# Performance work log

Measured on AMD Instinct MI355X. Metric: run time of the kernel, lower is better.

The kernel has to match this reference:

```python
import jax, jax.numpy as jnp
import numpy as np

N_VOX = 500_000
C = 128
HID = 4 * C
RES = 128  # voxel grid resolution
K_OFFS = 27


def _build_sparse_coords_and_neighbors(seed=0):
    rng = np.random.default_rng(seed)
    lin = rng.choice(RES ** 3, size=N_VOX, replace=False)
    z = lin // (RES * RES)
    y = (lin // RES) % RES
    x = lin % RES
    # padded grid (RES+2)^3 so boundary lookups are in-bounds
    P = RES + 2
    grid = -np.ones(P * P * P, dtype=np.int64)
    z1, y1, x1 = z + 1, y + 1, x + 1
    grid[z1 * P * P + y1 * P + x1] = np.arange(N_VOX)
    offs = np.array([[dz, dy, dx] for dz in (-1, 0, 1) for dy in (-1, 0, 1) for dx in (-1, 0, 1)], dtype=np.int64)  # [27,3]
    nz = z1[:, None] + offs[None, :, 0]
    ny = y1[:, None] + offs[None, :, 1]
    nx = x1[:, None] + offs[None, :, 2]
    nbr = grid[nz * P * P + ny * P + nx]  # [N,27], -1 if neighbor voxel inactive
    return nbr.astype(np.int32)


def setup_inputs() -> dict:
    key = jax.random.key(0)
    ks = jax.random.split(key, 8)
    nbr = _build_sparse_coords_and_neighbors()
    scale = 0.02
    return {
        "feats": jax.random.normal(ks[0], (N_VOX, C), jnp.float32),
        "neighbor_idx": jnp.asarray(nbr),
        "conv_w": jax.random.normal(ks[1], (K_OFFS, C, C), jnp.float32) * scale,
        "conv_b": jax.random.normal(ks[2], (C,), jnp.float32) * scale,
        "ln_g": jnp.ones((C,), jnp.float32),
        "ln_b": jnp.zeros((C,), jnp.float32),
        "w1": jax.random.normal(ks[3], (C, HID), jnp.float32) * scale,
        "b1": jax.random.normal(ks[4], (HID,), jnp.float32) * scale,
        "w2": jax.random.normal(ks[5], (HID, C), jnp.float32) * scale,
        "b2": jax.random.normal(ks[6], (C,), jnp.float32) * scale,
    }


def _forward(feats, neighbor_idx, conv_w, conv_b, ln_g, ln_b, w1, b1, w2, b2):
    n, c = feats.shape
    # submanifold sparse conv3d: pad a zero row for missing (-1) neighbors
    f_pad = jnp.concatenate([feats, jnp.zeros((1, c), feats.dtype)], axis=0)
    idx = jnp.where(neighbor_idx < 0, n, neighbor_idx)  # [N,27]
    h = jnp.broadcast_to(conv_b, (n, c))
    for k in range(K_OFFS):  # fixed small kernel-offset loop; per-offset gather + GEMM
        h = h + f_pad[idx[:, k]] @ conv_w[k]
    # LayerNorm32 (fp32 math), eps=1e-6, affine
    h32 = h.astype(jnp.float32)
    mu = h32.mean(-1, keepdims=True)
    var = h32.var(-1, keepdims=True)
    hn = ((h32 - mu) * jax.lax.rsqrt(var + 1e-6) * ln_g + ln_b).astype(feats.dtype)
    # MLP: Linear -> SiLU -> Linear
    m = jax.nn.silu(hn @ w1 + b1) @ w2 + b2
    # residual h + x on sparse feats
    return m + feats


def reference(feats, neighbor_idx, conv_w, conv_b, ln_g, ln_b, w1, b1, w2, b2):
    return _forward(feats, neighbor_idx, conv_w, conv_b, ln_g, ln_b, w1, b1, w2, b2)
```

## Files before the change

kernel.cpp:

```cpp
#include <hip/hip_runtime.h>
#include <stdint.h>

#define NVOX 500000
#define NPAD 500224
#define ZERO_OFF (NVOX * 128)

typedef float  f32x4  __attribute__((ext_vector_type(4)));
typedef short  short8 __attribute__((ext_vector_type(8)));

__device__ __forceinline__ short f2bf(float x){
  unsigned u = __float_as_uint(x);
  unsigned r = (u + 0x7fffu + ((u >> 16) & 1u)) >> 16;
  return (short)r;
}

__device__ __forceinline__ void gload_lds16(const void* g, void* l){
  __builtin_amdgcn_global_load_lds(
      (const __attribute__((address_space(1))) unsigned int*)(uintptr_t)g,
      (__attribute__((address_space(3))) unsigned int*)(unsigned int)(uintptr_t)l,
      16, 0, 0);
}

__global__ void cast_feats_kernel(const float* __restrict__ f, short* __restrict__ t){
  long i = ((long)blockIdx.x * 256 + threadIdx.x) * 8;
  float4 a = *(const float4*)(f + i);
  float4 b = *(const float4*)(f + i + 4);
  short8 o = { f2bf(a.x), f2bf(a.y), f2bf(a.z), f2bf(a.w),
               f2bf(b.x), f2bf(b.y), f2bf(b.z), f2bf(b.w) };
  *(short8*)(t + i) = o;
}

__global__ void prep_nbr_kernel(const int* __restrict__ nbr, int* __restrict__ nbrT){
  __shared__ int lds_n[6912];
  const int tid = threadIdx.x;
  const long base = (long)blockIdx.x * 6912;
  #pragma unroll
  for (int i = 0; i < 27; i++){
    long g = base + i*256 + tid;
    lds_n[i*256 + tid] = (g < (long)NVOX*27) ? nbr[g] : -1;
  }
  __syncthreads();
  const int row = blockIdx.x * 256 + tid;
  #pragma unroll
  for (int k = 0; k < 27; k++){
    int id = lds_n[tid*27 + k];
    nbrT[(size_t)k*NPAD + row] = (id < 0 ? NVOX : id) * 128;
  }
}

__global__ void prep_weights_kernel(const float* __restrict__ cw, const float* __restrict__ w1,
                                    const float* __restrict__ w2,
                                    short* __restrict__ cw_sw, short* __restrict__ w1_sw,
                                    short* __restrict__ w2_sw){
  int t = blockIdx.x * 256 + threadIdx.x;
  if (t < 55296){
    int k = t >> 11, rem = t & 2047;
    int nf = rem >> 8, ks = (rem >> 6) & 3, l = rem & 63;
    int g = l >> 4, c = l & 15;
    short8 o;
    #pragma unroll
    for (int j = 0; j < 8; j++){
      int kk = ks*32 + g*8 + j;
      o[j] = f2bf(cw[(k*128 + kk)*128 + nf*16 + c]);
    }
    *(short8*)(cw_sw + (size_t)t*8) = o;
  } else if (t < 63488){
    int u = t - 55296;
    int nf = u >> 8, ks = (u >> 6) & 3, l = u & 63;
    int g = l >> 4, c = l & 15;
    short8 o;
    #pragma unroll
    for (int j = 0; j < 8; j++){
      int kk = ks*32 + g*8 + j;
      o[j] = f2bf(w1[kk*512 + nf*16 + c]);
    }
    *(short8*)(w1_sw + (size_t)u*8) = o;
  } else {
    int u = t - 63488;
    int ch = u >> 10, rem = u & 1023;
    int nf = rem >> 7, ks2 = (rem >> 6) & 1, l = u & 63;
    int g = l >> 4, c = l & 15;
    short8 o;
    #pragma unroll
    for (int j = 0; j < 8; j++){
      int k = ch*64 + ks2*32 + g*8 + j;
      o[j] = f2bf(w2[k*128 + nf*16 + c]);
    }
    *(short8*)(w2_sw + (size_t)u*8) = o;
  }
}

__global__ __launch_bounds__(256, 2)
void conv_ln_pf_kernel(const short* __restrict__ table, const int* __restrict__ nbrT,
                       const short* __restrict__ cw_sw,
                       const float* __restrict__ conv_b, const float* __restrict__ ln_g,
                       const float* __restrict__ ln_b, short* __restrict__ hn16){
  __shared__ __align__(16) short lds_b[2][16384];
  const int tid = threadIdx.x;
  const int lane = tid & 63, wv = tid >> 6;
  const int l15 = lane & 15, lg = lane >> 4;
  const int rowbase = blockIdx.x * 256 + wv * 64;
  const int rowi = rowbase + l15;

  f32x4 acc[4][8];
  #pragma unroll
  for (int m = 0; m < 4; m++)
    #pragma unroll
    for (int n = 0; n < 8; n++)
      acc[m][n] = f32x4{0.f, 0.f, 0.f, 0.f};

  int idx_c[4], idx_n[4];
  #pragma unroll
  for (int m = 0; m < 4; m++) idx_c[m] = nbrT[rowi + m*16];
  #pragma unroll
  for (int m = 0; m < 4; m++) idx_n[m] = nbrT[NPAD + rowi + m*16];
  short8 afp[2][4];
  #pragma unroll
  for (int ks = 0; ks < 2; ks++)
    #pragma unroll
    for (int m = 0; m < 4; m++)
      afp[ks][m] = *(const short8*)(table + (size_t)(unsigned)idx_c[m] + ks*32 + lg*8);
  {
    const char* src = (const char*)cw_sw;
    char* dst = (char*)&lds_b[0][0];
    #pragma unroll
    for (int i = 0; i < 8; i++){ int off = i*4096 + tid*16; gload_lds16(src+off, dst+off); }
  }

  for (int k = 0; k < 27; k++){
    const int buf = k & 1;
    __syncthreads();
    short8 af2[4], af3[4];
    #pragma unroll
    for (int m = 0; m < 4; m++)
      af2[m] = *(const short8*)(table + (size_t)(unsigned)idx_c[m] + 64 + lg*8);
    #pragma unroll
    for (int m = 0; m < 4; m++)
      af3[m] = *(const short8*)(table + (size_t)(unsigned)idx_c[m] + 96 + lg*8);
    int idx_n2[4];
    #pragma unroll
    for (int m = 0; m < 4; m++)
      idx_n2[m] = (k + 2 < 27) ? nbrT[(size_t)(k+2)*NPAD + rowi + m*16] : ZERO_OFF;
    if (k + 1 < 27){
      const char* src = (const char*)cw_sw + (size_t)(k+1)*32768;
      char* dst = (char*)&lds_b[buf ^ 1][0];
      #pragma unroll
      for (int i = 0; i < 8; i++){ int off = i*4096 + tid*16; gload_lds16(src+off, dst+off); }
    }

    const short* bbase = &lds_b[buf][0];
    #pragma unroll
    for (int ks = 0; ks < 2; ks++){
      #pragma unroll
      for (int n = 0; n < 8; n++){
        short8 b = *(const short8*)(bbase + ((n*4 + ks)*64 + lane)*8);
        #pragma unroll
        for (int m = 0; m < 4; m++)
          acc[m][n] = __builtin_amdgcn_mfma_f32_16x16x32_bf16(afp[ks][m], b, acc[m][n], 0, 0, 0);
      }
    }
    short8 afp_n[2][4];
    #pragma unroll
    for (int ks = 0; ks < 2; ks++)
      #pragma unroll
      for (int m = 0; m < 4; m++)
        afp_n[ks][m] = *(const short8*)(table + (size_t)(unsigned)idx_n[m] + ks*32 + lg*8);
    #pragma unroll
    for (int n = 0; n < 8; n++){
      short8 b = *(const short8*)(bbase + ((n*4 + 2)*64 + lane)*8);
      #pragma unroll
      for (int m = 0; m < 4; m++)
        acc[m][n] = __builtin_amdgcn_mfma_f32_16x16x32_bf16(af2[m], b, acc[m][n], 0, 0, 0);
    }
    #pragma unroll
    for (int n = 0; n < 8; n++){
      short8 b = *(const short8*)(bbase + ((n*4 + 3)*64 + lane)*8);
      #pragma unroll
      for (int m = 0; m < 4; m++)
        acc[m][n] = __builtin_amdgcn_mfma_f32_16x16x32_bf16(af3[m], b, acc[m][n], 0, 0, 0);
    }
    #pragma unroll
    for (int m = 0; m < 4; m++){
      afp[0][m] = afp_n[0][m];
      afp[1][m] = afp_n[1][m];
      idx_c[m] = idx_n[m];
      idx_n[m] = idx_n2[m];
    }
  }

  float cb[8], g8[8], be[8];
  #pragma unroll
  for (int n = 0; n < 8; n++){
    cb[n] = conv_b[n*16 + l15];
    g8[n] = ln_g[n*16 + l15];
    be[n] = ln_b[n*16 + l15];
  }
  #pragma unroll
  for (int m = 0; m < 4; m++){
    #pragma unroll
    for (int r = 0; r < 4; r++){
      float s = 0.f, s2 = 0.f;
      #pragma unroll
      for (int n = 0; n < 8; n++){
        float h = acc[m][n][r] + cb[n];
        acc[m][n][r] = h;
        s += h; s2 += h*h;
      }
      #pragma unroll
      for (int msk = 1; msk < 16; msk <<= 1){
        s  += __shfl_xor(s,  msk);
        s2 += __shfl_xor(s2, msk);
      }
      float mu  = s  * 0.0078125f;
      float var = s2 * 0.0078125f - mu*mu;
      float rs  = rsqrtf(var + 1e-6f);
      int row = rowbase + m*16 + lg*4 + r;
      if (row < NVOX){
        #pragma unroll
        for (int n = 0; n < 8; n++){
          float hv = (acc[m][n][r] - mu) * rs * g8[n] + be[n];
          hn16[(size_t)row*128 + n*16 + l15] = f2bf(hv);
        }
      }
    }
  }
}

template<bool TBL>
__global__ __launch_bounds__(256, 2)
void conv_ln_kernel(const short* __restrict__ table, const float* __restrict__ feats,
                    const int* __restrict__ nbr, const short* __restrict__ cw_sw,
                    const float* __restrict__ conv_b, const float* __restrict__ ln_g,
                    const float* __restrict__ ln_b, short* __restrict__ hn16){
  __shared__ __align__(16) short lds_b[2][16384];
  const int tid = threadIdx.x;
  const int lane = tid & 63, wv = tid >> 6;
  const int l15 = lane & 15, lg = lane >> 4;
  const int rowbase = blockIdx.x * 256 + wv * 64;

  f32x4 acc[4][8];
  #pragma unroll
  for (int m = 0; m < 4; m++)
    #pragma unroll
    for (int n = 0; n < 8; n++)
      acc[m][n] = f32x4{0.f, 0.f, 0.f, 0.f};

  {
    const char* src = (const char*)cw_sw;
    char* dst = (char*)&lds_b[0][0];
    #pragma unroll
    for (int i = 0; i < 8; i++){ int off = i*4096 + tid*16; gload_lds16(src+off, dst+off); }
  }

  for (int k = 0; k < 27; k++){
    const int buf = k & 1;
    __syncthreads();
    if (k + 1 < 27){
      const char* src = (const char*)cw_sw + (size_t)(k+1)*32768;
      char* dst = (char*)&lds_b[buf ^ 1][0];
      #pragma unroll
      for (int i = 0; i < 8; i++){ int off = i*4096 + tid*16; gload_lds16(src+off, dst+off); }
    }
    int idxr[4];
    #pragma unroll
    for (int m = 0; m < 4; m++){
      int row = rowbase + m*16 + l15;
      row = row < NVOX ? row : NVOX - 1;
      int id = nbr[row*27 + k];
      idxr[m] = TBL ? (id < 0 ? NVOX : id) : id;
    }
    const short* bbase = &lds_b[buf][0];
    #pragma unroll
    for (int ks = 0; ks < 4; ks++){
      short8 af[4];
      #pragma unroll
      for (int m = 0; m < 4; m++){
        if constexpr (TBL){
          af[m] = *(const short8*)(table + (size_t)idxr[m]*128 + ks*32 + lg*8);
        } else {
          if (idxr[m] < 0){
            af[m] = short8{0,0,0,0,0,0,0,0};
          } else {
            const float* p = feats + (size_t)idxr[m]*128 + ks*32 + lg*8;
            float4 x = *(const float4*)p;
            float4 y = *(const float4*)(p + 4);
            af[m] = short8{ f2bf(x.x), f2bf(x.y), f2bf(x.z), f2bf(x.w),
                            f2bf(y.x), f2bf(y.y), f2bf(y.z), f2bf(y.w) };
          }
        }
      }
      #pragma unroll
      for (int n = 0; n < 8; n++){
        short8 b = *(const short8*)(bbase + ((n*4 + ks)*64 + lane)*8);
        #pragma unroll
        for (int m = 0; m < 4; m++)
          acc[m][n] = __builtin_amdgcn_mfma_f32_16x16x32_bf16(af[m], b, acc[m][n], 0, 0, 0);
      }
    }
  }

  float cb[8], g8[8], be[8];
  #pragma unroll
  for (int n = 0; n < 8; n++){
    cb[n] = conv_b[n*16 + l15];
    g8[n] = ln_g[n*16 + l15];
    be[n] = ln_b[n*16 + l15];
  }
  #pragma unroll
  for (int m = 0; m < 4; m++){
    #pragma unroll
    for (int r = 0; r < 4; r++){
      float s = 0.f, s2 = 0.f;
      #pragma unroll
      for (int n = 0; n < 8; n++){
        float h = acc[m][n][r] + cb[n];
        acc[m][n][r] = h;
        s += h; s2 += h*h;
      }
      #pragma unroll
      for (int msk = 1; msk < 16; msk <<= 1){
        s  += __shfl_xor(s,  msk);
        s2 += __shfl_xor(s2, msk);
      }
      float mu  = s  * 0.0078125f;
      float var = s2 * 0.0078125f - mu*mu;
      float rs  = rsqrtf(var + 1e-6f);
      int row = rowbase + m*16 + lg*4 + r;
      if (row < NVOX){
        #pragma unroll
        for (int n = 0; n < 8; n++){
          float hv = (acc[m][n][r] - mu) * rs * g8[n] + be[n];
          hn16[(size_t)row*128 + n*16 + l15] = f2bf(hv);
        }
      }
    }
  }
}

__global__ __launch_bounds__(256, 2)
void mlp_kernel(const short* __restrict__ hn16, const float* __restrict__ feats,
                const short* __restrict__ w1_sw, const short* __restrict__ w2_sw,
                const float* __restrict__ b1, const float* __restrict__ b2,
                float* __restrict__ out){
  __shared__ __align__(16) short lds_w[2][16384];
  __shared__ __align__(16) short lds_act[4*2048];
  const int tid = threadIdx.x;
  const int lane = tid & 63, wv = tid >> 6;
  const int l15 = lane & 15, lg = lane >> 4;
  const int rowbase = blockIdx.x * 128 + wv * 32;
  short* actw = &lds_act[wv * 2048];

  f32x4 acc2[2][8];
  #pragma unroll
  for (int m = 0; m < 2; m++)
    #pragma unroll
    for (int n = 0; n < 8; n++)
      acc2[m][n] = f32x4{0.f, 0.f, 0.f, 0.f};

  int rowg[2];
  #pragma unroll
  for (int m = 0; m < 2; m++){
    int row = rowbase + m*16 + l15;
    rowg[m] = row < NVOX ? row : NVOX - 1;
  }

  short8 a1[4][2];
  #pragma unroll
  for (int ks = 0; ks < 4; ks++)
    #pragma unroll
    for (int m = 0; m < 2; m++)
      a1[ks][m] = *(const short8*)(hn16 + (size_t)rowg[m]*128 + ks*32 + lg*8);

  {
    const char* s1 = (const char*)w1_sw;
    const char* s2 = (const char*)w2_sw;
    char* dst = (char*)&lds_w[0][0];
    #pragma unroll
    for (int i = 0; i < 4; i++){ int off = i*4096 + tid*16; gload_lds16(s1+off, dst+off); }
    #pragma unroll
    for (int i = 0; i < 4; i++){ int off = i*4096 + tid*16; gload_lds16(s2+off, dst+16384+off); }
  }

  for (int ch = 0; ch < 8; ch++){
    const int buf = ch & 1;
    __syncthreads();
    if (ch + 1 < 8){
      const char* s1 = (const char*)w1_sw + (size_t)(ch+1)*16384;
      const char* s2 = (const char*)w2_sw + (size_t)(ch+1)*16384;
      char* dst = (char*)&lds_w[buf ^ 1][0];
      #pragma unroll
      for (int i = 0; i < 4; i++){ int off = i*4096 + tid*16; gload_lds16(s1+off, dst+off); }
      #pragma unroll
      for (int i = 0; i < 4; i++){ int off = i*4096 + tid*16; gload_lds16(s2+off, dst+16384+off); }
    }
    const short* w1c = &lds_w[buf][0];
    const short* w2c = &lds_w[buf][8192];

    #pragma unroll
    for (int n = 0; n < 4; n++){
      f32x4 p0 = f32x4{0.f,0.f,0.f,0.f};
      f32x4 p1 = f32x4{0.f,0.f,0.f,0.f};
      #pragma unroll
      for (int ks = 0; ks < 4; ks++){
        short8 b = *(const short8*)(w1c + ((n*4 + ks)*64 + lane)*8);
        p0 = __builtin_amdgcn_mfma_f32_16x16x32_bf16(a1[ks][0], b, p0, 0, 0, 0);
        p1 = __builtin_amdgcn_mfma_f32_16x16x32_bf16(a1[ks][1], b, p1, 0, 0, 0);
      }
      float bb1 = b1[ch*64 + n*16 + l15];
      #pragma unroll
      for (int r = 0; r < 4; r++){
        float x0 = p0[r] + bb1;
        float x1 = p1[r] + bb1;
        float s0 = x0 / (1.f + __expf(-x0));
        float s1 = x1 / (1.f + __expf(-x1));
        int r0 = lg*4 + r;
        int r1 = 16 + lg*4 + r;
        actw[(r0*64 + n*16 + l15) ^ ((r0 & 7) << 3)] = f2bf(s0);
        actw[(r1*64 + n*16 + l15) ^ ((r1 & 7) << 3)] = f2bf(s1);
      }
    }

    #pragma unroll
    for (int ks2 = 0; ks2 < 2; ks2++){
      short8 a2[2];
      #pragma unroll
      for (int m = 0; m < 2; m++){
        int rowloc = m*16 + l15;
        a2[m] = *(const short8*)(actw + ((rowloc*64 + ks2*32 + lg*8) ^ ((rowloc & 7) << 3)));
      }
      #pragma unroll
      for (int n = 0; n < 8; n++){
        short8 b = *(const short8*)(w2c + ((n*2 + ks2)*64 + lane)*8);
        #pragma unroll
        for (int m = 0; m < 2; m++)
          acc2[m][n] = __builtin_amdgcn_mfma_f32_16x16x32_bf16(a2[m], b, acc2[m][n], 0, 0, 0);
      }
    }
  }

  float bb2[8];
  #pragma unroll
  for (int n = 0; n < 8; n++) bb2[n] = b2[n*16 + l15];
  #pragma unroll
  for (int m = 0; m < 2; m++)
    #pragma unroll
    for (int n = 0; n < 8; n++)
      #pragma unroll
      for (int r = 0; r < 4; r++){
        int row = rowbase + m*16 + lg*4 + r;
        if (row < NVOX){
          size_t ci = (size_t)row*128 + n*16 + l15;
          out[ci] = acc2[m][n][r] + bb2[n] + feats[ci];
        }
      }
}

extern "C" void kernel_launch(void* const* d_in, const int* in_sizes, int n_in,
                              void* d_out, int out_size, void* d_ws, size_t ws_size,
                              hipStream_t stream){
  const float* feats = (const float*)d_in[0];
  const int*   nbr   = (const int*)  d_in[1];
  const float* cw    = (const float*)d_in[2];
  const float* cb    = (const float*)d_in[3];
  const float* lng   = (const float*)d_in[4];
  const float* lnb   = (const float*)d_in[5];
  const float* w1    = (const float*)d_in[6];
  const float* b1    = (const float*)d_in[7];
  const float* w2    = (const float*)d_in[8];
  const float* b2    = (const float*)d_in[9];
  float* out = (float*)d_out;

  char* ws = (char*)d_ws;
  const size_t TABLE_B = (size_t)(NVOX + 1) * 256;
  const size_t HN_B    = (size_t)NVOX * 256;
  const size_t CW_B    = 55296u * 16u;
  const size_t W1_B    = 8192u * 16u;
  const size_t W2_B    = 8192u * 16u;
  const size_t NBRT_B  = (size_t)27 * NPAD * 4;
  const size_t need_full = TABLE_B + HN_B + CW_B + W1_B + W2_B;
  const size_t need_pf   = need_full + NBRT_B;

  if (ws_size >= need_pf){
    short* table = (short*)ws;
    short* hn16  = (short*)(ws + TABLE_B);
    short* cw_sw = (short*)(ws + TABLE_B + HN_B);
    short* w1_sw = (short*)(ws + TABLE_B + HN_B + CW_B);
    short* w2_sw = (short*)(ws + TABLE_B + HN_B + CW_B + W1_B);
    int*   nbrT  = (int*)  (ws + need_full);

    cast_feats_kernel<<<31250, 256, 0, stream>>>(feats, table);
    hipMemsetAsync((void*)(table + (size_t)NVOX * 128), 0, 256, stream);
    prep_nbr_kernel<<<1954, 256, 0, stream>>>(nbr, nbrT);
    prep_weights_kernel<<<280, 256, 0, stream>>>(cw, w1, w2, cw_sw, w1_sw, w2_sw);
    conv_ln_pf_kernel<<<1954, 256, 0, stream>>>(table, nbrT, cw_sw, cb, lng, lnb, hn16);
    mlp_kernel<<<3907, 256, 0, stream>>>(hn16, feats, w1_sw, w2_sw, b1, b2, out);
  } else if (ws_size >= need_full){
    short* table = (short*)ws;
    short* hn16  = (short*)(ws + TABLE_B);
    short* cw_sw = (short*)(ws + TABLE_B + HN_B);
    short* w1_sw = (short*)(ws + TABLE_B + HN_B + CW_B);
    short* w2_sw = (short*)(ws + TABLE_B + HN_B + CW_B + W1_B);

    cast_feats_kernel<<<31250, 256, 0, stream>>>(feats, table);
    hipMemsetAsync((void*)(table + (size_t)NVOX * 128), 0, 256, stream);
    prep_weights_kernel<<<280, 256, 0, stream>>>(cw, w1, w2, cw_sw, w1_sw, w2_sw);
    conv_ln_kernel<true><<<1954, 256, 0, stream>>>(table, feats, nbr, cw_sw, cb, lng, lnb, hn16);
    mlp_kernel<<<3907, 256, 0, stream>>>(hn16, feats, w1_sw, w2_sw, b1, b2, out);
  } else {
    short* hn16  = (short*)ws;
    short* cw_sw = (short*)(ws + HN_B);
    short* w1_sw = (short*)(ws + HN_B + CW_B);
    short* w2_sw = (short*)(ws + HN_B + CW_B + W1_B);

    prep_weights_kernel<<<280, 256, 0, stream>>>(cw, w1, w2, cw_sw, w1_sw, w2_sw);
    conv_ln_kernel<false><<<1954, 256, 0, stream>>>(nullptr, feats, nbr, cw_sw, cb, lng, lnb, hn16);
    mlp_kernel<<<3907, 256, 0, stream>>>(hn16, feats, w1_sw, w2_sw, b1, b2, out);
  }
}
```

Baseline: 929.8 us.

## Split conv tile across wave pairs, halve LDS, raise occupancy

The conv+LayerNorm kernel now uses 128-row blocks, and two waves split the 128 output channels of each 64-row slab. This halves the accumulator registers and lets launch bounds request 4 blocks per CU. The weights are re-laid out into 16 KB half-offset chunks, so each offset is streamed in two halves through a 2x8192-short LDS buffer. LayerNorm row statistics are combined across the wave pair through shared memory. In exchange, every neighbour row is gathered twice (once per column half), the cross-offset A prefetch is dropped, and there are extra barriers per offset.

```diff
diff --git a/kernel.cpp b/kernel.cpp
--- a/kernel.cpp
+++ b/kernel.cpp
@@ -63,7 +63,8 @@
       int kk = ks*32 + g*8 + j;
       o[j] = f2bf(cw[(k*128 + kk)*128 + nf*16 + c]);
     }
-    *(short8*)(cw_sw + (size_t)t*8) = o;
+    size_t dst = (size_t)(k*2 + (ks >> 1))*8192 + (size_t)(nf*2 + (ks & 1))*512 + (size_t)l*8;
+    *(short8*)(cw_sw + dst) = o;
   } else if (t < 63488){
     int u = t - 55296;
     int nf = u >> 8, ks = (u >> 6) & 3, l = u & 63;
@@ -90,23 +91,26 @@
   }
 }
 
-__global__ __launch_bounds__(256, 2)
-void conv_ln_pf_kernel(const short* __restrict__ table, const int* __restrict__ nbrT,
+__global__ __launch_bounds__(256, 4)
+void conv_ln_v3_kernel(const short* __restrict__ table, const int* __restrict__ nbrT,
                        const short* __restrict__ cw_sw,
                        const float* __restrict__ conv_b, const float* __restrict__ ln_g,
                        const float* __restrict__ ln_b, short* __restrict__ hn16){
-  __shared__ __align__(16) short lds_b[2][16384];
+  __shared__ __align__(16) short lds_b[2][8192];
+  __shared__ float lds_s[128][2];
+  __shared__ float lds_s2[128][2];
   const int tid = threadIdx.x;
   const int lane = tid & 63, wv = tid >> 6;
+  const int wr = wv >> 1, wc = wv & 1;
   const int l15 = lane & 15, lg = lane >> 4;
-  const int rowbase = blockIdx.x * 256 + wv * 64;
+  const int rowbase = blockIdx.x * 128 + wr * 64;
   const int rowi = rowbase + l15;
 
-  f32x4 acc[4][8];
+  f32x4 acc[4][4];
   #pragma unroll
   for (int m = 0; m < 4; m++)
     #pragma unroll
-    for (int n = 0; n < 8; n++)
+    for (int n = 0; n < 4; n++)
       acc[m][n] = f32x4{0.f, 0.f, 0.f, 0.f};
 
   int idx_c[4], idx_n[4];
@@ -114,21 +118,46 @@
   for (int m = 0; m < 4; m++) idx_c[m] = nbrT[rowi + m*16];
   #pragma unroll
   for (int m = 0; m < 4; m++) idx_n[m] = nbrT[NPAD + rowi + m*16];
-  short8 afp[2][4];
-  #pragma unroll
-  for (int ks = 0; ks < 2; ks++)
-    #pragma unroll
-    for (int m = 0; m < 4; m++)
-      afp[ks][m] = *(const short8*)(table + (size_t)(unsigned)idx_c[m] + ks*32 + lg*8);
+
   {
     const char* src = (const char*)cw_sw;
     char* dst = (char*)&lds_b[0][0];
     #pragma unroll
-    for (int i = 0; i < 8; i++){ int off = i*4096 + tid*16; gload_lds16(src+off, dst+off); }
+    for (int i = 0; i < 4; i++){ int off = i*4096 + tid*16; gload_lds16(src+off, dst+off); }
   }
 
   for (int k = 0; k < 27; k++){
-    const int buf = k & 1;
+    __syncthreads();
+    short8 af0[4], af1[4];
+    #pragma unroll
+    for (int m = 0; m < 4; m++)
+      af0[m] = *(const short8*)(table + (size_t)(unsigned)idx_c[m] + lg*8);
+    #pragma unroll
+    for (int m = 0; m < 4; m++)
+      af1[m] = *(const short8*)(table + (size_t)(unsigned)idx_c[m] + 32 + lg*8);
+    {
+      const char* src = (const char*)cw_sw + (size_t)(k*2 + 1)*16384;
+      char* dst = (char*)&lds_b[1][0];
+      #pragma unroll
+      for (int i = 0; i < 4; i++){ int off = i*4096 + tid*16; gload_lds16(src+off, dst+off); }
+    }
+    {
+      const short* b0 = &lds_b[0][0];
+      #pragma unroll
+      for (int n = 0; n < 4; n++){
+        short8 b = *(const short8*)(b0 + (((wc*4 + n)*2 + 0)*64 + lane)*8);
+        #pragma unroll
+        for (int m = 0; m < 4; m++)
+          acc[m][n] = __builtin_amdgcn_mfma_f32_16x16x32_bf16(af0[m], b, acc[m][n], 0, 0, 0);
+      }
+      #pragma unroll
+      for (int n = 0; n < 4; n++){
+        short8 b = *(const short8*)(b0 + (((wc*4 + n)*2 + 1)*64 + lane)*8);
+        #pragma unroll
+        for (int m = 0; m < 4; m++)
+          acc[m][n] = __builtin_amdgcn_mfma_f32_16x16x32_bf16(af1[m], b, acc[m][n], 0, 0, 0);
+      }
+    }
     __syncthreads();
     short8 af2[4], af3[4];
     #pragma unroll
@@ -137,63 +166,43 @@
     #pragma unroll
     for (int m = 0; m < 4; m++)
       af3[m] = *(const short8*)(table + (size_t)(unsigned)idx_c[m] + 96 + lg*8);
+    if (k + 1 < 27){
+      const char* src = (const char*)cw_sw + (size_t)(k+1)*32768;
+      char* dst = (char*)&lds_b[0][0];
+      #pragma unroll
+      for (int i = 0; i < 4; i++){ int off = i*4096 + tid*16; gload_lds16(src+off, dst+off); }
+    }
     int idx_n2[4];
     #pragma unroll
     for (int m = 0; m < 4; m++)
       idx_n2[m] = (k + 2 < 27) ? nbrT[(size_t)(k+2)*NPAD + rowi + m*16] : ZERO_OFF;
-    if (k + 1 < 27){
-      const char* src = (const char*)cw_sw + (size_t)(k+1)*32768;
-      char* dst = (char*)&lds_b[buf ^ 1][0];
-      #pragma unroll
-      for (int i = 0; i < 8; i++){ int off = i*4096 + tid*16; gload_lds16(src+off, dst+off); }
-    }
-
-    const short* bbase = &lds_b[buf][0];
-    #pragma unroll
-    for (int ks = 0; ks < 2; ks++){
-      #pragma unroll
-      for (int n = 0; n < 8; n++){
-        short8 b = *(const short8*)(bbase + ((n*4 + ks)*64 + lane)*8);
+    {
+      const short* b1 = &lds_b[1][0];
+      #pragma unroll
+      for (int n = 0; n < 4; n++){
+        short8 b = *(const short8*)(b1 + (((wc*4 + n)*2 + 0)*64 + lane)*8);
         #pragma unroll
         for (int m = 0; m < 4; m++)
-          acc[m][n] = __builtin_amdgcn_mfma_f32_16x16x32_bf16(afp[ks][m], b, acc[m][n], 0, 0, 0);
-      }
-    }
-    short8 afp_n[2][4];
-    #pragma unroll
-    for (int ks = 0; ks < 2; ks++)
-      #pragma unroll
-      for (int m = 0; m < 4; m++)
-        afp_n[ks][m] = *(const short8*)(table + (size_t)(unsigned)idx_n[m] + ks*32 + lg*8);
-    #pragma unroll
-    for (int n = 0; n < 8; n++){
-      short8 b = *(const short8*)(bbase + ((n*4 + 2)*64 + lane)*8);
-      #pragma unroll
-      for (int m = 0; m < 4; m++)
-        acc[m][n] = __builtin_amdgcn_mfma_f32_16x16x32_bf16(af2[m], b, acc[m][n], 0, 0, 0);
-    }
-    #pragma unroll
-    for (int n = 0; n < 8; n++){
-      short8 b = *(const short8*)(bbase + ((n*4 + 3)*64 + lane)*8);
-      #pragma unroll
-      for (int m = 0; m < 4; m++)
-        acc[m][n] = __builtin_amdgcn_mfma_f32_16x16x32_bf16(af3[m], b, acc[m][n], 0, 0, 0);
-    }
-    #pragma unroll
-    for (int m = 0; m < 4; m++){
-      afp[0][m] = afp_n[0][m];
-      afp[1][m] = afp_n[1][m];
-      idx_c[m] = idx_n[m];
-      idx_n[m] = idx_n2[m];
-    }
-  }
-
-  float cb[8], g8[8], be[8];
-  #pragma unroll
-  for (int n = 0; n < 8; n++){
-    cb[n] = conv_b[n*16 + l15];
-    g8[n] = ln_g[n*16 + l15];
-    be[n] = ln_b[n*16 + l15];
+          acc[m][n] = __builtin_amdgcn_mfma_f32_16x16x32_bf16(af2[m], b, acc[m][n], 0, 0, 0);
+      }
+      #pragma unroll
+      for (int n = 0; n < 4; n++){
+        short8 b = *(const short8*)(b1 + (((wc*4 + n)*2 + 1)*64 + lane)*8);
+        #pragma unroll
+        for (int m = 0; m < 4; m++)
+          acc[m][n] = __builtin_amdgcn_mfma_f32_16x16x32_bf16(af3[m], b, acc[m][n], 0, 0, 0);
+      }
+    }
+    #pragma unroll
+    for (int m = 0; m < 4; m++){ idx_c[m] = idx_n[m]; idx_n[m] = idx_n2[m]; }
+  }
+
+  float cb[4], g4[4], be[4];
+  #pragma unroll
+  for (int n = 0; n < 4; n++){
+    cb[n] = conv_b[wc*64 + n*16 + l15];
+    g4[n] = ln_g[wc*64 + n*16 + l15];
+    be[n] = ln_b[wc*64 + n*16 + l15];
   }
   #pragma unroll
   for (int m = 0; m < 4; m++){
@@ -201,7 +210,7 @@
     for (int r = 0; r < 4; r++){
       float s = 0.f, s2 = 0.f;
       #pragma unroll
-      for (int n = 0; n < 8; n++){
+      for (int n = 0; n < 4; n++){
         float h = acc[m][n][r] + cb[n];
         acc[m][n][r] = h;
         s += h; s2 += h*h;
@@ -211,15 +220,27 @@
         s  += __shfl_xor(s,  msk);
         s2 += __shfl_xor(s2, msk);
       }
+      int rl = wr*64 + m*16 + lg*4 + r;
+      if (l15 == 0){ lds_s[rl][wc] = s; lds_s2[rl][wc] = s2; }
+    }
+  }
+  __syncthreads();
+  #pragma unroll
+  for (int m = 0; m < 4; m++){
+    #pragma unroll
+    for (int r = 0; r < 4; r++){
+      int rl = wr*64 + m*16 + lg*4 + r;
+      float s  = lds_s[rl][0]  + lds_s[rl][1];
+      float s2 = lds_s2[rl][0] + lds_s2[rl][1];
       float mu  = s  * 0.0078125f;
       float var = s2 * 0.0078125f - mu*mu;
       float rs  = rsqrtf(var + 1e-6f);
-      int row = rowbase + m*16 + lg*4 + r;
+      int row = blockIdx.x * 128 + rl;
       if (row < NVOX){
         #pragma unroll
-        for (int n = 0; n < 8; n++){
-          float hv = (acc[m][n][r] - mu) * rs * g8[n] + be[n];
-          hn16[(size_t)row*128 + n*16 + l15] = f2bf(hv);
+        for (int n = 0; n < 4; n++){
+          float hv = (acc[m][n][r] - mu) * rs * g4[n] + be[n];
+          hn16[(size_t)row*128 + wc*64 + n*16 + l15] = f2bf(hv);
         }
       }
     }
@@ -291,7 +312,7 @@
       }
       #pragma unroll
       for (int n = 0; n < 8; n++){
-        short8 b = *(const short8*)(bbase + ((n*4 + ks)*64 + lane)*8);
+        short8 b = *(const short8*)(bbase + (ks >> 1)*8192 + (((n*2 + (ks & 1))*64) + lane)*8);
         #pragma unroll
         for (int m = 0; m < 4; m++)
           acc[m][n] = __builtin_amdgcn_mfma_f32_16x16x32_bf16(af[m], b, acc[m][n], 0, 0, 0);
@@ -492,7 +513,7 @@
     hipMemsetAsync((void*)(table + (size_t)NVOX * 128), 0, 256, stream);
     prep_nbr_kernel<<<1954, 256, 0, stream>>>(nbr, nbrT);
     prep_weights_kernel<<<280, 256, 0, stream>>>(cw, w1, w2, cw_sw, w1_sw, w2_sw);
-    conv_ln_pf_kernel<<<1954, 256, 0, stream>>>(table, nbrT, cw_sw, cb, lng, lnb, hn16);
+    conv_ln_v3_kernel<<<3907, 256, 0, stream>>>(table, nbrT, cw_sw, cb, lng, lnb, hn16);
     mlp_kernel<<<3907, 256, 0, stream>>>(hn16, feats, w1_sw, w2_sw, b1, b2, out);
   } else if (ws_size >= need_full){
     short* table = (short*)ws;
```

After: 1.234 ms. 32.7% more time.

## Stream MLP weights from global into registers instead of LDS double buffering

Applied to the files above, without the earlier changes.

The MLP kernel stops staging W1/W2 chunks in shared memory with per-chunk __syncthreads. Each wave now loads its MFMA B fragments directly from global memory (L2-resident) into registers, prefetching the next fragment one step ahead. Hidden chunks grow from 64 to 128 columns, which doubles the per-wave activation LDS buffer and halves the chunk loop count. This removes block-wide barriers and cuts LDS use, which may raise occupancy. In exchange every wave issues redundant global loads for the weights and carries more registers for the prefetch buffers.

```diff
diff --git a/kernel.cpp b/kernel.cpp
--- a/kernel.cpp
+++ b/kernel.cpp
@@ -342,13 +342,12 @@
                 const short* __restrict__ w1_sw, const short* __restrict__ w2_sw,
                 const float* __restrict__ b1, const float* __restrict__ b2,
                 float* __restrict__ out){
-  __shared__ __align__(16) short lds_w[2][16384];
-  __shared__ __align__(16) short lds_act[4*2048];
+  __shared__ __align__(16) short lds_act[4*4096];
   const int tid = threadIdx.x;
   const int lane = tid & 63, wv = tid >> 6;
   const int l15 = lane & 15, lg = lane >> 4;
   const int rowbase = blockIdx.x * 128 + wv * 32;
-  short* actw = &lds_act[wv * 2048];
+  short* actw = &lds_act[wv * 4096];
 
   f32x4 acc2[2][8];
   #pragma unroll
@@ -371,42 +370,26 @@
     for (int m = 0; m < 2; m++)
       a1[ks][m] = *(const short8*)(hn16 + (size_t)rowg[m]*128 + ks*32 + lg*8);
 
-  {
-    const char* s1 = (const char*)w1_sw;
-    const char* s2 = (const char*)w2_sw;
-    char* dst = (char*)&lds_w[0][0];
-    #pragma unroll
-    for (int i = 0; i < 4; i++){ int off = i*4096 + tid*16; gload_lds16(s1+off, dst+off); }
-    #pragma unroll
-    for (int i = 0; i < 4; i++){ int off = i*4096 + tid*16; gload_lds16(s2+off, dst+16384+off); }
-  }
-
-  for (int ch = 0; ch < 8; ch++){
-    const int buf = ch & 1;
-    __syncthreads();
-    if (ch + 1 < 8){
-      const char* s1 = (const char*)w1_sw + (size_t)(ch+1)*16384;
-      const char* s2 = (const char*)w2_sw + (size_t)(ch+1)*16384;
-      char* dst = (char*)&lds_w[buf ^ 1][0];
-      #pragma unroll
-      for (int i = 0; i < 4; i++){ int off = i*4096 + tid*16; gload_lds16(s1+off, dst+off); }
-      #pragma unroll
-      for (int i = 0; i < 4; i++){ int off = i*4096 + tid*16; gload_lds16(s2+off, dst+16384+off); }
-    }
-    const short* w1c = &lds_w[buf][0];
-    const short* w2c = &lds_w[buf][8192];
-
-    #pragma unroll
-    for (int n = 0; n < 4; n++){
+  for (int ch = 0; ch < 4; ch++){
+    short8 bw[4], bn[4];
+    #pragma unroll
+    for (int ks = 0; ks < 4; ks++)
+      bw[ks] = *(const short8*)(w1_sw + (size_t)((ch*8 + 0)*4 + ks)*512 + lane*8);
+    #pragma unroll
+    for (int nf = 0; nf < 8; nf++){
+      if (nf < 7){
+        #pragma unroll
+        for (int ks = 0; ks < 4; ks++)
+          bn[ks] = *(const short8*)(w1_sw + (size_t)((ch*8 + nf + 1)*4 + ks)*512 + lane*8);
+      }
       f32x4 p0 = f32x4{0.f,0.f,0.f,0.f};
       f32x4 p1 = f32x4{0.f,0.f,0.f,0.f};
       #pragma unroll
       for (int ks = 0; ks < 4; ks++){
-        short8 b = *(const short8*)(w1c + ((n*4 + ks)*64 + lane)*8);
-        p0 = __builtin_amdgcn_mfma_f32_16x16x32_bf16(a1[ks][0], b, p0, 0, 0, 0);
-        p1 = __builtin_amdgcn_mfma_f32_16x16x32_bf16(a1[ks][1], b, p1, 0, 0, 0);
-      }
-      float bb1 = b1[ch*64 + n*16 + l15];
+        p0 = __builtin_amdgcn_mfma_f32_16x16x32_bf16(a1[ks][0], bw[ks], p0, 0, 0, 0);
+        p1 = __builtin_amdgcn_mfma_f32_16x16x32_bf16(a1[ks][1], bw[ks], p1, 0, 0, 0);
+      }
+      float bb1 = b1[ch*128 + nf*16 + l15];
       #pragma unroll
       for (int r = 0; r < 4; r++){
         float x0 = p0[r] + bb1;
@@ -415,26 +398,43 @@
         float s1 = x1 / (1.f + __expf(-x1));
         int r0 = lg*4 + r;
         int r1 = 16 + lg*4 + r;
-        actw[(r0*64 + n*16 + l15) ^ ((r0 & 7) << 3)] = f2bf(s0);
-        actw[(r1*64 + n*16 + l15) ^ ((r1 & 7) << 3)] = f2bf(s1);
-      }
-    }
-
-    #pragma unroll
-    for (int ks2 = 0; ks2 < 2; ks2++){
-      short8 a2[2];
+        actw[(r0*128 + nf*16 + l15) ^ ((r0 & 7) << 3)] = f2bf(s0);
+        actw[(r1*128 + nf*16 + l15) ^ ((r1 & 7) << 3)] = f2bf(s1);
+      }
+      #pragma unroll
+      for (int ks = 0; ks < 4; ks++) bw[ks] = bn[ks];
+    }
+
+    short8 a2h[4][2];
+    #pragma unroll
+    for (int ks2 = 0; ks2 < 4; ks2++)
       #pragma unroll
       for (int m = 0; m < 2; m++){
         int rowloc = m*16 + l15;
-        a2[m] = *(const short8*)(actw + ((rowloc*64 + ks2*32 + lg*8) ^ ((rowloc & 7) << 3)));
-      }
-      #pragma unroll
-      for (int n = 0; n < 8; n++){
-        short8 b = *(const short8*)(w2c + ((n*2 + ks2)*64 + lane)*8);
+        a2h[ks2][m] = *(const short8*)(actw + ((rowloc*128 + ks2*32 + lg*8) ^ ((rowloc & 7) << 3)));
+      }
+    short8 cw[4], cn[4];
+    #pragma unroll
+    for (int ks2 = 0; ks2 < 4; ks2++){
+      int ch64 = ch*2 + (ks2 >> 1), kk = ks2 & 1;
+      cw[ks2] = *(const short8*)(w2_sw + (size_t)(((ch64*8 + 0)*2 + kk)*64 + lane)*8);
+    }
+    #pragma unroll
+    for (int nfo = 0; nfo < 8; nfo++){
+      if (nfo < 7){
         #pragma unroll
-        for (int m = 0; m < 2; m++)
-          acc2[m][n] = __builtin_amdgcn_mfma_f32_16x16x32_bf16(a2[m], b, acc2[m][n], 0, 0, 0);
-      }
+        for (int ks2 = 0; ks2 < 4; ks2++){
+          int ch64 = ch*2 + (ks2 >> 1), kk = ks2 & 1;
+          cn[ks2] = *(const short8*)(w2_sw + (size_t)(((ch64*8 + nfo + 1)*2 + kk)*64 + lane)*8);
+        }
+      }
+      #pragma unroll
+      for (int ks2 = 0; ks2 < 4; ks2++){
+        acc2[0][nfo] = __builtin_amdgcn_mfma_f32_16x16x32_bf16(a2h[ks2][0], cw[ks2], acc2[0][nfo], 0, 0, 0);
+        acc2[1][nfo] = __builtin_amdgcn_mfma_f32_16x16x32_bf16(a2h[ks2][1], cw[ks2], acc2[1][nfo], 0, 0, 0);
+      }
+      #pragma unroll
+      for (int ks2 = 0; ks2 < 4; ks2++) cw[ks2] = cn[ks2];
     }
   }
 
```

New measurement: 1.027 ms. +10.4%, slower.

## Double MLP rows per wave and single-buffer weight chunks in LDS

Applied to the files above, without the earlier changes.

Each wave in the MLP kernel now processes 64 rows instead of 32, so every weight fragment read from LDS feeds four MFMAs instead of two. The grid is halved to match. The double-buffered weight prefetch is replaced by a single buffer loaded and then waited on with a barrier each chunk, which frees LDS for the larger activation tile. The cost is more registers per thread (more accumulators and a larger A tile), possible occupancy loss, and the weight loads no longer overlapping with compute.

```diff
diff --git a/kernel.cpp b/kernel.cpp
--- a/kernel.cpp
+++ b/kernel.cpp
@@ -342,97 +342,86 @@
                 const short* __restrict__ w1_sw, const short* __restrict__ w2_sw,
                 const float* __restrict__ b1, const float* __restrict__ b2,
                 float* __restrict__ out){
-  __shared__ __align__(16) short lds_w[2][16384];
-  __shared__ __align__(16) short lds_act[4*2048];
+  __shared__ __align__(16) short lds_w[16384];
+  __shared__ __align__(16) short lds_act[4*4096];
   const int tid = threadIdx.x;
   const int lane = tid & 63, wv = tid >> 6;
   const int l15 = lane & 15, lg = lane >> 4;
-  const int rowbase = blockIdx.x * 128 + wv * 32;
-  short* actw = &lds_act[wv * 2048];
-
-  f32x4 acc2[2][8];
-  #pragma unroll
-  for (int m = 0; m < 2; m++)
+  const int rowbase = blockIdx.x * 256 + wv * 64;
+  short* actw = &lds_act[wv * 4096];
+
+  f32x4 acc2[4][8];
+  #pragma unroll
+  for (int m = 0; m < 4; m++)
     #pragma unroll
     for (int n = 0; n < 8; n++)
       acc2[m][n] = f32x4{0.f, 0.f, 0.f, 0.f};
 
-  int rowg[2];
-  #pragma unroll
-  for (int m = 0; m < 2; m++){
+  int rowg[4];
+  #pragma unroll
+  for (int m = 0; m < 4; m++){
     int row = rowbase + m*16 + l15;
     rowg[m] = row < NVOX ? row : NVOX - 1;
   }
 
-  short8 a1[4][2];
+  short8 a1[4][4];
   #pragma unroll
   for (int ks = 0; ks < 4; ks++)
     #pragma unroll
-    for (int m = 0; m < 2; m++)
+    for (int m = 0; m < 4; m++)
       a1[ks][m] = *(const short8*)(hn16 + (size_t)rowg[m]*128 + ks*32 + lg*8);
 
-  {
-    const char* s1 = (const char*)w1_sw;
-    const char* s2 = (const char*)w2_sw;
-    char* dst = (char*)&lds_w[0][0];
-    #pragma unroll
-    for (int i = 0; i < 4; i++){ int off = i*4096 + tid*16; gload_lds16(s1+off, dst+off); }
-    #pragma unroll
-    for (int i = 0; i < 4; i++){ int off = i*4096 + tid*16; gload_lds16(s2+off, dst+16384+off); }
-  }
-
   for (int ch = 0; ch < 8; ch++){
-    const int buf = ch & 1;
     __syncthreads();
-    if (ch + 1 < 8){
-      const char* s1 = (const char*)w1_sw + (size_t)(ch+1)*16384;
-      const char* s2 = (const char*)w2_sw + (size_t)(ch+1)*16384;
-      char* dst = (char*)&lds_w[buf ^ 1][0];
+    {
+      const char* s1 = (const char*)w1_sw + (size_t)ch*16384;
+      const char* s2 = (const char*)w2_sw + (size_t)ch*16384;
+      char* dst = (char*)lds_w;
       #pragma unroll
       for (int i = 0; i < 4; i++){ int off = i*4096 + tid*16; gload_lds16(s1+off, dst+off); }
       #pragma unroll
       for (int i = 0; i < 4; i++){ int off = i*4096 + tid*16; gload_lds16(s2+off, dst+16384+off); }
     }
-    const short* w1c = &lds_w[buf][0];
-    const short* w2c = &lds_w[buf][8192];
-
-    #pragma unroll
-    for (int n = 0; n < 4; n++){
-      f32x4 p0 = f32x4{0.f,0.f,0.f,0.f};
-      f32x4 p1 = f32x4{0.f,0.f,0.f,0.f};
+    __syncthreads();
+
+    #pragma unroll
+    for (int nf = 0; nf < 4; nf++){
+      f32x4 p[4];
+      #pragma unroll
+      for (int m = 0; m < 4; m++) p[m] = f32x4{0.f,0.f,0.f,0.f};
       #pragma unroll
       for (int ks = 0; ks < 4; ks++){
-        short8 b = *(const short8*)(w1c + ((n*4 + ks)*64 + lane)*8);
-        p0 = __builtin_amdgcn_mfma_f32_16x16x32_bf16(a1[ks][0], b, p0, 0, 0, 0);
-        p1 = __builtin_amdgcn_mfma_f32_16x16x32_bf16(a1[ks][1], b, p1, 0, 0, 0);
-      }
-      float bb1 = b1[ch*64 + n*16 + l15];
-      #pragma unroll
-      for (int r = 0; r < 4; r++){
-        float x0 = p0[r] + bb1;
-        float x1 = p1[r] + bb1;
-        float s0 = x0 / (1.f + __expf(-x0));
-        float s1 = x1 / (1.f + __expf(-x1));
-        int r0 = lg*4 + r;
-        int r1 = 16 + lg*4 + r;
-        actw[(r0*64 + n*16 + l15) ^ ((r0 & 7) << 3)] = f2bf(s0);
-        actw[(r1*64 + n*16 + l15) ^ ((r1 & 7) << 3)] = f2bf(s1);
+        short8 b = *(const short8*)(lds_w + ((nf*4 + ks)*64 + lane)*8);
+        #pragma unroll
+        for (int m = 0; m < 4; m++)
+          p[m] = __builtin_amdgcn_mfma_f32_16x16x32_bf16(a1[ks][m], b, p[m], 0, 0, 0);
+      }
+      float bb1 = b1[ch*64 + nf*16 + l15];
+      #pragma unroll
+      for (int m = 0; m < 4; m++){
+        #pragma unroll
+        for (int r = 0; r < 4; r++){
+          float x = p[m][r] + bb1;
+          float sg = x / (1.f + __expf(-x));
+          int rowloc = m*16 + lg*4 + r;
+          actw[(rowloc*64 + nf*16 + l15) ^ ((rowloc & 7) << 3)] = f2bf(sg);
+        }
       }
     }
 
     #pragma unroll
     for (int ks2 = 0; ks2 < 2; ks2++){
-      short8 a2[2];
-      #pragma unroll
-      for (int m = 0; m < 2; m++){
+      short8 a2[4];
+      #pragma unroll
+      for (int m = 0; m < 4; m++){
         int rowloc = m*16 + l15;
         a2[m] = *(const short8*)(actw + ((rowloc*64 + ks2*32 + lg*8) ^ ((rowloc & 7) << 3)));
       }
       #pragma unroll
       for (int n = 0; n < 8; n++){
-        short8 b = *(const short8*)(w2c + ((n*2 + ks2)*64 + lane)*8);
-        #pragma unroll
-        for (int m = 0; m < 2; m++)
+        short8 b = *(const short8*)(lds_w + 8192 + ((n*2 + ks2)*64 + lane)*8);
+        #pragma unroll
+        for (int m = 0; m < 4; m++)
           acc2[m][n] = __builtin_amdgcn_mfma_f32_16x16x32_bf16(a2[m], b, acc2[m][n], 0, 0, 0);
       }
     }
@@ -442,7 +431,7 @@
   #pragma unroll
   for (int n = 0; n < 8; n++) bb2[n] = b2[n*16 + l15];
   #pragma unroll
-  for (int m = 0; m < 2; m++)
+  for (int m = 0; m < 4; m++)
     #pragma unroll
     for (int n = 0; n < 8; n++)
       #pragma unroll
@@ -493,7 +482,7 @@
     prep_nbr_kernel<<<1954, 256, 0, stream>>>(nbr, nbrT);
     prep_weights_kernel<<<280, 256, 0, stream>>>(cw, w1, w2, cw_sw, w1_sw, w2_sw);
     conv_ln_pf_kernel<<<1954, 256, 0, stream>>>(table, nbrT, cw_sw, cb, lng, lnb, hn16);
-    mlp_kernel<<<3907, 256, 0, stream>>>(hn16, feats, w1_sw, w2_sw, b1, b2, out);
+    mlp_kernel<<<1954, 256, 0, stream>>>(hn16, feats, w1_sw, w2_sw, b1, b2, out);
   } else if (ws_size >= need_full){
     short* table = (short*)ws;
     short* hn16  = (short*)(ws + TABLE_B);
@@ -505,7 +494,7 @@
     hipMemsetAsync((void*)(table + (size_t)NVOX * 128), 0, 256, stream);
     prep_weights_kernel<<<280, 256, 0, stream>>>(cw, w1, w2, cw_sw, w1_sw, w2_sw);
     conv_ln_kernel<true><<<1954, 256, 0, stream>>>(table, feats, nbr, cw_sw, cb, lng, lnb, hn16);
-    mlp_kernel<<<3907, 256, 0, stream>>>(hn16, feats, w1_sw, w2_sw, b1, b2, out);
+    mlp_kernel<<<1954, 256, 0, stream>>>(hn16, feats, w1_sw, w2_sw, b1, b2, out);
   } else {
     short* hn16  = (short*)ws;
     short* cw_sw = (short*)(ws + HN_B);
@@ -514,6 +503,6 @@
 
     prep_weights_kernel<<<280, 256, 0, stream>>>(cw, w1, w2, cw_sw, w1_sw, w2_sw);
     conv_ln_kernel<false><<<1954, 256, 0, stream>>>(nullptr, feats, nbr, cw_sw, cb, lng, lnb, hn16);
-    mlp_kernel<<<3907, 256, 0, stream>>>(hn16, feats, w1_sw, w2_sw, b1, b2, out);
-  }
-}
+    mlp_kernel<<<1954, 256, 0, stream>>>(hn16, feats, w1_sw, w2_sw, b1, b2, out);
+  }
+}
```

After: 1.179 ms. 26.9% more time.
